# Kernel optimization log

Measured on AMD Instinct MI355X. Metric: run time of the kernel, lower is better.

## Reference

```python
import jax, jax.numpy as jnp
import numpy as np

N_NODES = 100_000
N_EDGES = 3_200_000
IN_CH = 128
HID = 64


def setup_inputs() -> dict:
    key = jax.random.key(0)
    k0, k1, k2, k3 = jax.random.split(key, 4)
    x = jax.random.normal(k0, (N_NODES, IN_CH), dtype=jnp.float32)
    edge_index = jax.random.randint(k1, (2, N_EDGES), 0, N_NODES)
    # GCNConv internal linear (no bias) -> W1; separate additive bias b1
    W1 = jax.random.normal(k2, (HID, IN_CH), dtype=jnp.float32) * 0.05
    b1 = jnp.zeros((HID,), dtype=jnp.float32)
    W2 = jax.random.normal(k3, (1, HID), dtype=jnp.float32) * 0.05
    b2 = jnp.zeros((1,), dtype=jnp.float32)
    return {"x": x, "edge_index": edge_index, "W1": W1, "b1": b1, "W2": W2, "b2": b2}


def reference(x, edge_index, W1, b1, W2, b2):
    n = x.shape[0]
    # --- GCNConv: add self-loops, symmetric degree normalization ---
    loops = jnp.arange(n, dtype=edge_index.dtype)
    src = jnp.concatenate([edge_index[0], loops])  # [E+N]
    dst = jnp.concatenate([edge_index[1], loops])  # [E+N]
    deg = jax.ops.segment_sum(jnp.ones_like(dst, dtype=x.dtype), dst, num_segments=n)
    dinv = jnp.where(deg > 0, jax.lax.rsqrt(deg), 0.0)
    norm = dinv[src] * dinv[dst]                   # [E+N]
    h = x @ W1.T                                   # [N, HID]
    msg = h[src] * norm[:, None]                   # [E+N, HID] gather
    agg = jax.ops.segment_sum(msg, dst, num_segments=n) + b1  # scatter-add
    # --- ReLU + Linear(hidden, 1) + squeeze ---
    out = jax.nn.relu(agg) @ W2.T + b2             # [N, 1]
    return out.squeeze(-1)
```

## Files before the change

kernel.cpp:

```cpp
#include <hip/hip_runtime.h>
#include <hip/hip_bf16.h>


typedef unsigned int u32;
typedef unsigned short u16;
typedef __attribute__((ext_vector_type(8))) short bf16x8;
typedef __attribute__((ext_vector_type(4))) float f32x4;

#define PK 4096
#define PTH 512
#define EPT (PK/PTH)
#define CAPB 9216

__device__ __forceinline__ short f2bf(float f) {
    __hip_bfloat16 h = __float2bfloat16(f);
    return *reinterpret_cast<short*>(&h);
}
__device__ __forceinline__ float bf2f(u16 u) {
    return __uint_as_float(((u32)u) << 16);
}
__device__ __forceinline__ bf16x8 pack8(float4 lo, float4 hi) {
    bf16x8 o;
    o[0] = f2bf(lo.x); o[1] = f2bf(lo.y); o[2] = f2bf(lo.z); o[3] = f2bf(lo.w);
    o[4] = f2bf(hi.x); o[5] = f2bf(hi.y); o[6] = f2bf(hi.z); o[7] = f2bf(hi.w);
    return o;
}

__global__ __launch_bounds__(512) void setup_kernel(int* __restrict__ bcnt,
                                                    const float* __restrict__ W1,
                                                    u16* __restrict__ wbf, int NB) {
    int t = threadIdx.x;
    if (blockIdx.x == 0) {
        if (t < NB) bcnt[t] = 0;
    } else {
#pragma unroll
        for (int i = 0; i < 16; ++i) wbf[i * 512 + t] = (u16)f2bf(W1[i * 512 + t]);
    }
}

__global__ __launch_bounds__(PTH) void part_kernel(const int* __restrict__ src,
                                                   const int* __restrict__ dst,
                                                   int* __restrict__ bcnt,
                                                   u32* __restrict__ ebuf, int E, int NB) {
    __shared__ u32 stage[PK];
    __shared__ u16 sbid[PK];
    __shared__ int h[512], loff[512], gbase[512], cur[512];
    int t = threadIdx.x;
    int e0 = blockIdx.x * PK;
    int e1 = e0 + PK; if (e1 > E) e1 = E;
    int cnt = e1 - e0;
    h[t] = 0; cur[t] = 0;
    __syncthreads();
    int dreg[EPT];
#pragma unroll
    for (int i = 0; i < EPT; ++i) {
        int e = e0 + i * PTH + t;
        dreg[i] = (e < e1) ? dst[e] : -1;
        if (dreg[i] >= 0) atomicAdd(&h[dreg[i] >> 8], 1);
    }
    __syncthreads();
    if (t < 64) {
        int carry = 0;
        for (int c = 0; c < 8; ++c) {
            int idx = c * 64 + t;
            int v = h[idx], incl = v;
            for (int d2 = 1; d2 < 64; d2 <<= 1) {
                int o = __shfl_up(incl, d2);
                if (t >= d2) incl += o;
            }
            loff[idx] = carry + incl - v;
            carry += __shfl(incl, 63);
        }
    }
    __syncthreads();
    if (t < NB) {
        int bb = t + (blockIdx.x % NB);
        if (bb >= NB) bb -= NB;
        gbase[bb] = bb * CAPB + atomicAdd(&bcnt[bb], h[bb]);
    }
    __syncthreads();
#pragma unroll
    for (int i = 0; i < EPT; ++i) {
        int d = dreg[i];
        if (d >= 0) {
            int e = e0 + i * PTH + t;
            int s = src[e];
            int bk = d >> 8;
            int r = atomicAdd(&cur[bk], 1);
            int p = loff[bk] + r;
            stage[p] = ((u32)(d & 255) << 17) | (u32)s;
            sbid[p] = (u16)bk;
        }
    }
    __syncthreads();
    for (int i = t; i < cnt; i += PTH) {
        int bk = sbid[i];
        ebuf[gbase[bk] + (i - loff[bk])] = stage[i];
    }
}

__global__ __launch_bounds__(512) void csrg_kernel(u32* ebuf,
                                                   const int* __restrict__ bcnt,
                                                   int* __restrict__ offs,
                                                   int* __restrict__ degc,
                                                   const float* __restrict__ x,
                                                   const u16* __restrict__ wbf,
                                                   u16* __restrict__ gb,
                                                   int N) {
    __shared__ u32 stage[CAPB];
    __shared__ int h2[256], lofs[256], cur2[256];
    int t = threadIdx.x;
    int b = blockIdx.x;
    int base = b << 8;
    int e0 = b * CAPB;
    int cnt = bcnt[b];
    if (cnt > CAPB) cnt = CAPB;
    if (t < 256) { h2[t] = 0; cur2[t] = 0; }
    __syncthreads();
    for (int e = t; e < cnt; e += 512) atomicAdd(&h2[(int)(ebuf[e0 + e] >> 17)], 1);
    __syncthreads();
    if (t < 64) {
        int carry = 0;
        for (int c = 0; c < 4; ++c) {
            int idx = c * 64 + t;
            int v = h2[idx], incl = v;
            for (int d2 = 1; d2 < 64; d2 <<= 1) {
                int o = __shfl_up(incl, d2);
                if (t >= d2) incl += o;
            }
            lofs[idx] = carry + incl - v;
            carry += __shfl(incl, 63);
        }
    }
    __syncthreads();
    if (t < 256) {
        int n = base + t;
        if (n < N) { offs[n] = e0 + lofs[t]; degc[n] = h2[t]; }
    }

    int lane = t & 63;
    int wv = t >> 6;
    int r = lane & 15;
    int g = lane >> 4;
#pragma unroll
    for (int it = 0; it < 2; ++it) {
        int n0 = base + (it * 8 + wv) * 16;
        int nr = n0 + r; if (nr >= N) nr = N - 1;
        const float* xrow = x + (size_t)nr * 128 + g * 8;
        bf16x8 afr[4];
#pragma unroll
        for (int ks = 0; ks < 4; ++ks) {
            float4 lo = *(const float4*)(xrow + ks * 32);
            float4 hi = *(const float4*)(xrow + ks * 32 + 4);
            afr[ks] = pack8(lo, hi);
        }
        f32x4 acc[4] = {f32x4{0.f,0.f,0.f,0.f}, f32x4{0.f,0.f,0.f,0.f},
                        f32x4{0.f,0.f,0.f,0.f}, f32x4{0.f,0.f,0.f,0.f}};
#pragma unroll
        for (int ct = 0; ct < 4; ++ct) {
            const u16* wrow = wbf + (ct * 16 + r) * 128 + g * 8;
#pragma unroll
            for (int ks = 0; ks < 4; ++ks) {
                bf16x8 bfr = *(const bf16x8*)(wrow + ks * 32);
                acc[ct] = __builtin_amdgcn_mfma_f32_16x16x32_bf16(afr[ks], bfr, acc[ct], 0, 0, 0);
            }
        }
#pragma unroll
        for (int reg = 0; reg < 4; ++reg) {
            int n = n0 + g * 4 + reg;
            if (n < N) {
                int dl = n - base;
                float dv = rsqrtf((float)(h2[dl] + 1));
#pragma unroll
                for (int ct = 0; ct < 4; ++ct)
                    gb[(size_t)n * 64 + ct * 16 + r] = (u16)f2bf(dv * acc[ct][reg]);
            }
        }
    }

    for (int e = t; e < cnt; e += 512) {
        u32 pk = ebuf[e0 + e];
        int dl = (int)(pk >> 17);
        int rr = atomicAdd(&cur2[dl], 1);
        stage[lofs[dl] + rr] = pk & 0x1FFFF;
    }
    __syncthreads();
    for (int e = t; e < cnt; e += 512) ebuf[e0 + e] = stage[e];
}

__global__ __launch_bounds__(256) void agg_kernel(const u16* __restrict__ gb,
                                                  const int* __restrict__ csr,
                                                  const int* __restrict__ offs,
                                                  const int* __restrict__ degc,
                                                  const float* __restrict__ W2,
                                                  const float* __restrict__ b1,
                                                  const float* __restrict__ b2,
                                                  float* __restrict__ out, int N) {
    int wid = blockIdx.x * 4 + (threadIdx.x >> 6);
    int lane = threadIdx.x & 63;
    if (wid >= N) return;
    int off = __builtin_amdgcn_readfirstlane(offs[wid]);
    int cnt = __builtin_amdgcn_readfirstlane(degc[wid]);
    const u16* gbl = gb + lane;
    float acc = bf2f(gbl[(size_t)wid * 64]);
    int j = 0;
    for (; j + 16 <= cnt; j += 16) {
        float v[16];
#pragma unroll
        for (int k = 0; k < 16; ++k) {
            int s = csr[off + j + k];
            v[k] = bf2f(gbl[(size_t)s * 64]);
        }
        float s01 = (v[0] + v[1]) + (v[2] + v[3]);
        float s23 = (v[4] + v[5]) + (v[6] + v[7]);
        float s45 = (v[8] + v[9]) + (v[10] + v[11]);
        float s67 = (v[12] + v[13]) + (v[14] + v[15]);
        acc += (s01 + s23) + (s45 + s67);
    }
    for (; j + 4 <= cnt; j += 4) {
        float v[4];
#pragma unroll
        for (int k = 0; k < 4; ++k) {
            int s = csr[off + j + k];
            v[k] = bf2f(gbl[(size_t)s * 64]);
        }
        acc += (v[0] + v[1]) + (v[2] + v[3]);
    }
    for (; j < cnt; ++j) {
        int s = csr[off + j];
        acc += bf2f(gbl[(size_t)s * 64]);
    }
    float dv = rsqrtf((float)(cnt + 1));
    float val = fmaxf(dv * acc + b1[lane], 0.f) * W2[lane];
#pragma unroll
    for (int o = 32; o >= 1; o >>= 1) val += __shfl_xor(val, o);
    if (lane == 0) out[wid] = val + b2[0];
}

extern "C" void kernel_launch(void* const* d_in, const int* in_sizes, int n_in,
                              void* d_out, int out_size, void* d_ws, size_t ws_size,
                              hipStream_t stream) {
    const float* x  = (const float*)d_in[0];
    const int*   ei = (const int*)d_in[1];
    const float* W1 = (const float*)d_in[2];
    const float* b1 = (const float*)d_in[3];
    const float* W2 = (const float*)d_in[4];
    const float* b2 = (const float*)d_in[5];
    float* out = (float*)d_out;

    int N = in_sizes[0] / 128;
    int E = in_sizes[1] / 2;
    const int* src = ei;
    const int* dst = ei + E;
    int NB = (N + 255) >> 8;
    int NBLK = (E + PK - 1) / PK;

    char* ws = (char*)d_ws;
    int* bcnt = (int*)(ws + 0x000000);
    int* degc = (int*)(ws + 0x010000);
    int* offs = (int*)(ws + 0x080000);
    u16* wbf  = (u16*)(ws + 0x0F0000);
    u32* ebuf = (u32*)(ws + 0x100000);
    u16* gb   = (u16*)(ws + 0xF80000);

    setup_kernel<<<2, 512, 0, stream>>>(bcnt, W1, wbf, NB);
    part_kernel<<<NBLK, PTH, 0, stream>>>(src, dst, bcnt, ebuf, E, NB);
    csrg_kernel<<<NB, 512, 0, stream>>>(ebuf, bcnt, offs, degc, x, wbf, gb, N);
    agg_kernel<<<(N + 3) / 4, 256, 0, stream>>>(gb, (const int*)ebuf, offs, degc, W2, b1, b2, out, N);
}
```

Baseline: 135.7 us.

## Halve CSR bucket size and split dense GEMM into its own kernel

Destination buckets shrink from 256 to 128 nodes, which doubles the number of CSR-build blocks (about 782 instead of 391) and roughly halves their shared-memory staging, so more blocks can be resident and the GPU is better filled. The X·W1 MFMA GEMM moves out of the CSR-build kernel into a separate kernel with 64-row tiles. That kernel converts W1 to bf16 on the fly, so the setup kernel is replaced by a memset. The cost is one extra launch, a larger partition histogram per block (1024 bins), and a tighter per-bucket capacity that gives less headroom for skewed degree distributions.

```diff
diff --git a/kernel.cpp b/kernel.cpp
--- a/kernel.cpp
+++ b/kernel.cpp
@@ -10,7 +10,8 @@
 #define PK 4096
 #define PTH 512
 #define EPT (PK/PTH)
-#define CAPB 9216
+#define NBMAX 1024
+#define CAPB 4864
 
 __device__ __forceinline__ short f2bf(float f) {
     __hip_bfloat16 h = __float2bfloat16(f);
@@ -24,18 +25,6 @@
     o[0] = f2bf(lo.x); o[1] = f2bf(lo.y); o[2] = f2bf(lo.z); o[3] = f2bf(lo.w);
     o[4] = f2bf(hi.x); o[5] = f2bf(hi.y); o[6] = f2bf(hi.z); o[7] = f2bf(hi.w);
     return o;
-}
-
-__global__ __launch_bounds__(512) void setup_kernel(int* __restrict__ bcnt,
-                                                    const float* __restrict__ W1,
-                                                    u16* __restrict__ wbf, int NB) {
-    int t = threadIdx.x;
-    if (blockIdx.x == 0) {
-        if (t < NB) bcnt[t] = 0;
-    } else {
-#pragma unroll
-        for (int i = 0; i < 16; ++i) wbf[i * 512 + t] = (u16)f2bf(W1[i * 512 + t]);
-    }
 }
 
 __global__ __launch_bounds__(PTH) void part_kernel(const int* __restrict__ src,
@@ -44,24 +33,24 @@
                                                    u32* __restrict__ ebuf, int E, int NB) {
     __shared__ u32 stage[PK];
     __shared__ u16 sbid[PK];
-    __shared__ int h[512], loff[512], gbase[512], cur[512];
+    __shared__ int h[NBMAX], loff[NBMAX], gbase[NBMAX], cur[NBMAX];
     int t = threadIdx.x;
     int e0 = blockIdx.x * PK;
     int e1 = e0 + PK; if (e1 > E) e1 = E;
     int cnt = e1 - e0;
-    h[t] = 0; cur[t] = 0;
+    for (int i = t; i < NBMAX; i += PTH) { h[i] = 0; cur[i] = 0; }
     __syncthreads();
     int dreg[EPT];
 #pragma unroll
     for (int i = 0; i < EPT; ++i) {
         int e = e0 + i * PTH + t;
         dreg[i] = (e < e1) ? dst[e] : -1;
-        if (dreg[i] >= 0) atomicAdd(&h[dreg[i] >> 8], 1);
+        if (dreg[i] >= 0) atomicAdd(&h[dreg[i] >> 7], 1);
     }
     __syncthreads();
     if (t < 64) {
         int carry = 0;
-        for (int c = 0; c < 8; ++c) {
+        for (int c = 0; c < 16; ++c) {
             int idx = c * 64 + t;
             int v = h[idx], incl = v;
             for (int d2 = 1; d2 < 64; d2 <<= 1) {
@@ -73,10 +62,12 @@
         }
     }
     __syncthreads();
-    if (t < NB) {
-        int bb = t + (blockIdx.x % NB);
-        if (bb >= NB) bb -= NB;
-        gbase[bb] = bb * CAPB + atomicAdd(&bcnt[bb], h[bb]);
+    {
+        int rot = blockIdx.x % NB;
+        for (int b0 = t; b0 < NB; b0 += PTH) {
+            int bb = b0 + rot; if (bb >= NB) bb -= NB;
+            gbase[bb] = bb * CAPB + atomicAdd(&bcnt[bb], h[bb]);
+        }
     }
     __syncthreads();
 #pragma unroll
@@ -85,10 +76,10 @@
         if (d >= 0) {
             int e = e0 + i * PTH + t;
             int s = src[e];
-            int bk = d >> 8;
+            int bk = d >> 7;
             int r = atomicAdd(&cur[bk], 1);
             int p = loff[bk] + r;
-            stage[p] = ((u32)(d & 255) << 17) | (u32)s;
+            stage[p] = ((u32)(d & 127) << 17) | (u32)s;
             sbid[p] = (u16)bk;
         }
     }
@@ -99,29 +90,26 @@
     }
 }
 
-__global__ __launch_bounds__(512) void csrg_kernel(u32* ebuf,
+__global__ __launch_bounds__(512) void csrb_kernel(u32* ebuf,
                                                    const int* __restrict__ bcnt,
                                                    int* __restrict__ offs,
                                                    int* __restrict__ degc,
-                                                   const float* __restrict__ x,
-                                                   const u16* __restrict__ wbf,
-                                                   u16* __restrict__ gb,
                                                    int N) {
     __shared__ u32 stage[CAPB];
-    __shared__ int h2[256], lofs[256], cur2[256];
+    __shared__ int h2[128], lofs[128], cur2[128];
     int t = threadIdx.x;
     int b = blockIdx.x;
-    int base = b << 8;
+    int base = b << 7;
     int e0 = b * CAPB;
     int cnt = bcnt[b];
     if (cnt > CAPB) cnt = CAPB;
-    if (t < 256) { h2[t] = 0; cur2[t] = 0; }
+    if (t < 128) { h2[t] = 0; cur2[t] = 0; }
     __syncthreads();
     for (int e = t; e < cnt; e += 512) atomicAdd(&h2[(int)(ebuf[e0 + e] >> 17)], 1);
     __syncthreads();
     if (t < 64) {
         int carry = 0;
-        for (int c = 0; c < 4; ++c) {
+        for (int c = 0; c < 2; ++c) {
             int idx = c * 64 + t;
             int v = h2[idx], incl = v;
             for (int d2 = 1; d2 < 64; d2 <<= 1) {
@@ -133,59 +121,65 @@
         }
     }
     __syncthreads();
-    if (t < 256) {
+    if (t < 128) {
         int n = base + t;
         if (n < N) { offs[n] = e0 + lofs[t]; degc[n] = h2[t]; }
     }
-
-    int lane = t & 63;
-    int wv = t >> 6;
-    int r = lane & 15;
-    int g = lane >> 4;
-#pragma unroll
-    for (int it = 0; it < 2; ++it) {
-        int n0 = base + (it * 8 + wv) * 16;
-        int nr = n0 + r; if (nr >= N) nr = N - 1;
-        const float* xrow = x + (size_t)nr * 128 + g * 8;
-        bf16x8 afr[4];
-#pragma unroll
-        for (int ks = 0; ks < 4; ++ks) {
-            float4 lo = *(const float4*)(xrow + ks * 32);
-            float4 hi = *(const float4*)(xrow + ks * 32 + 4);
-            afr[ks] = pack8(lo, hi);
-        }
-        f32x4 acc[4] = {f32x4{0.f,0.f,0.f,0.f}, f32x4{0.f,0.f,0.f,0.f},
-                        f32x4{0.f,0.f,0.f,0.f}, f32x4{0.f,0.f,0.f,0.f}};
-#pragma unroll
-        for (int ct = 0; ct < 4; ++ct) {
-            const u16* wrow = wbf + (ct * 16 + r) * 128 + g * 8;
-#pragma unroll
-            for (int ks = 0; ks < 4; ++ks) {
-                bf16x8 bfr = *(const bf16x8*)(wrow + ks * 32);
-                acc[ct] = __builtin_amdgcn_mfma_f32_16x16x32_bf16(afr[ks], bfr, acc[ct], 0, 0, 0);
-            }
-        }
-#pragma unroll
-        for (int reg = 0; reg < 4; ++reg) {
-            int n = n0 + g * 4 + reg;
-            if (n < N) {
-                int dl = n - base;
-                float dv = rsqrtf((float)(h2[dl] + 1));
-#pragma unroll
-                for (int ct = 0; ct < 4; ++ct)
-                    gb[(size_t)n * 64 + ct * 16 + r] = (u16)f2bf(dv * acc[ct][reg]);
-            }
-        }
-    }
-
     for (int e = t; e < cnt; e += 512) {
         u32 pk = ebuf[e0 + e];
         int dl = (int)(pk >> 17);
-        int rr = atomicAdd(&cur2[dl], 1);
-        stage[lofs[dl] + rr] = pk & 0x1FFFF;
+        int r = atomicAdd(&cur2[dl], 1);
+        stage[lofs[dl] + r] = pk & 0x1FFFF;
     }
     __syncthreads();
     for (int e = t; e < cnt; e += 512) ebuf[e0 + e] = stage[e];
+}
+
+__global__ __launch_bounds__(256) void gemm_kernel(const float* __restrict__ x,
+                                                   const float* __restrict__ W1,
+                                                   const int* __restrict__ degc,
+                                                   u16* __restrict__ gb, int N) {
+    int t = threadIdx.x;
+    int lane = t & 63;
+    int wv = t >> 6;
+    int n0 = blockIdx.x * 64 + wv * 16;
+    int r = lane & 15;
+    int g = lane >> 4;
+
+    int nr = n0 + r; if (nr >= N) nr = N - 1;
+    const float* xrow = x + (size_t)nr * 128 + g * 8;
+    bf16x8 afr[4];
+#pragma unroll
+    for (int ks = 0; ks < 4; ++ks) {
+        float4 lo = *(const float4*)(xrow + ks * 32);
+        float4 hi = *(const float4*)(xrow + ks * 32 + 4);
+        afr[ks] = pack8(lo, hi);
+    }
+
+    f32x4 acc[4] = {f32x4{0.f,0.f,0.f,0.f}, f32x4{0.f,0.f,0.f,0.f},
+                    f32x4{0.f,0.f,0.f,0.f}, f32x4{0.f,0.f,0.f,0.f}};
+#pragma unroll
+    for (int ct = 0; ct < 4; ++ct) {
+        const float* wrow = W1 + (size_t)(ct * 16 + r) * 128 + g * 8;
+#pragma unroll
+        for (int ks = 0; ks < 4; ++ks) {
+            float4 wlo = *(const float4*)(wrow + ks * 32);
+            float4 whi = *(const float4*)(wrow + ks * 32 + 4);
+            bf16x8 bfr = pack8(wlo, whi);
+            acc[ct] = __builtin_amdgcn_mfma_f32_16x16x32_bf16(afr[ks], bfr, acc[ct], 0, 0, 0);
+        }
+    }
+
+#pragma unroll
+    for (int reg = 0; reg < 4; ++reg) {
+        int n = n0 + g * 4 + reg;
+        if (n < N) {
+            float dv = rsqrtf((float)(degc[n] + 1));
+#pragma unroll
+            for (int ct = 0; ct < 4; ++ct)
+                gb[(size_t)n * 64 + ct * 16 + r] = (u16)f2bf(dv * acc[ct][reg]);
+        }
+    }
 }
 
 __global__ __launch_bounds__(256) void agg_kernel(const u16* __restrict__ gb,
@@ -252,19 +246,19 @@
     int E = in_sizes[1] / 2;
     const int* src = ei;
     const int* dst = ei + E;
-    int NB = (N + 255) >> 8;
+    int NB = (N + 127) >> 7;
     int NBLK = (E + PK - 1) / PK;
 
     char* ws = (char*)d_ws;
     int* bcnt = (int*)(ws + 0x000000);
     int* degc = (int*)(ws + 0x010000);
     int* offs = (int*)(ws + 0x080000);
-    u16* wbf  = (u16*)(ws + 0x0F0000);
     u32* ebuf = (u32*)(ws + 0x100000);
-    u16* gb   = (u16*)(ws + 0xF80000);
-
-    setup_kernel<<<2, 512, 0, stream>>>(bcnt, W1, wbf, NB);
+    u16* gb   = (u16*)(ws + 0x1000000);
+
+    hipMemsetAsync(bcnt, 0, (size_t)NB * 4, stream);
     part_kernel<<<NBLK, PTH, 0, stream>>>(src, dst, bcnt, ebuf, E, NB);
-    csrg_kernel<<<NB, 512, 0, stream>>>(ebuf, bcnt, offs, degc, x, wbf, gb, N);
+    csrb_kernel<<<NB, 512, 0, stream>>>(ebuf, bcnt, offs, degc, N);
+    gemm_kernel<<<(N + 63) / 64, 256, 0, stream>>>(x, W1, degc, gb, N);
     agg_kernel<<<(N + 3) / 4, 256, 0, stream>>>(gb, (const int*)ebuf, offs, degc, W2, b1, b2, out, N);
 }
```

After: 150.0 us. 1.11x slower.
